# Kernel tuning notes

Hardware: AMD Instinct MI355X
Metric: run time of the kernel (lower is better)

Reference implementation:

```python
import jax, jax.numpy as jnp
import numpy as np

EPS = 1e-07

def setup_inputs() -> dict:
    key = jax.random.key(0)
    kx, kw, kb, ku = jax.random.split(key, 4)
    B, S, D, A = 1024, 512, 200, 100
    x = jax.random.normal(kx, (B, S, D), dtype=jnp.float32)
    W = jax.random.normal(kw, (D, A), dtype=jnp.float32)
    b = jax.random.normal(kb, (A,), dtype=jnp.float32)
    u = jax.random.normal(ku, (A, 1), dtype=jnp.float32)
    return {"x": x, "W": W, "b": b, "u": u}

def reference(x, W, b, u):
    # uit: [B,S,A] = tanh(x @ W + b)
    uit = jnp.tanh(jnp.einsum('bsd,da->bsa', x, W) + b)
    # ait: [B,S] raw scores -> exp -> normalize over seq (faithful: no max-subtract)
    ait = jnp.exp(jnp.einsum('bsa,a->bs', uit, u[:, 0]))
    ait = ait / (jnp.sum(ait, axis=1, keepdims=True) + EPS)
    # weighted sum pool over seq: [B,D]
    return jnp.einsum('bsd,bs->bd', x, ait)
```

## Files before the change

kernel.cpp:

```cpp
#include <hip/hip_runtime.h>
#include <math.h>


typedef _Float16 half8 __attribute__((ext_vector_type(8)));
typedef _Float16 half4_ __attribute__((ext_vector_type(4)));
typedef float float4_ __attribute__((ext_vector_type(4)));

#define B_   1024
#define S_   512
#define D_   200
#define A_   100
#define NPAD 128
#define KPAD 224
#define SC   64
#define NCH  (S_ / SC)
#define PITCH_H 232

#define WT_BYTES (NPAD * KPAD * 2)
#define UB_BYTES (NPAD * 2 * 4)
#define NUM_OFF  (WT_BYTES + UB_BYTES)
#define DEN_OFF  (NUM_OFF + (size_t)B_ * NCH * 4 * D_ * 4)

#define DPP_ADD(v, ctrl)                                                     \
  v += __builtin_bit_cast(float, __builtin_amdgcn_update_dpp(                \
           0, __builtin_bit_cast(int, v), (ctrl), 0xF, 0xF, true))

__global__ void prep_kernel(const float* __restrict__ W,
                            const float* __restrict__ bias,
                            const float* __restrict__ u,
                            void* __restrict__ ws) {
  _Float16* wt = (_Float16*)ws;
  float* upad = (float*)((char*)ws + WT_BYTES);
  float* bpad = upad + NPAD;
  int idx = blockIdx.x * 256 + threadIdx.x;
  if (idx < NPAD * KPAD) {
    int n = idx / KPAD;
    int k = idx % KPAD;
    float v = (n < A_ && k < D_) ? W[k * A_ + n] : 0.f;
    wt[idx] = (_Float16)v;
  }
  if (blockIdx.x == 0 && threadIdx.x < NPAD) {
    int t = threadIdx.x;
    upad[t] = (t < A_) ? u[t] : 0.f;
    bpad[t] = (t < A_) ? bias[t] : 0.f;
  }
}

__global__ __launch_bounds__(256, 4)
void attn_kernel(const float* __restrict__ x,
                 void* __restrict__ ws) {
  __shared__ _Float16 xs[SC * PITCH_H];
  __shared__ float score_part[4][SC];
  __shared__ float e_lds[SC];

  const int blk  = blockIdx.x;
  const int b    = blk >> 3;
  const int chunk= blk & 7;
  const int tid  = threadIdx.x;
  const int lane = tid & 63;
  const int wave = tid >> 6;
  const int lm   = lane & 15;
  const int lq   = lane >> 4;

  const _Float16* wt = (const _Float16*)ws;
  const float* upad = (const float*)((const char*)ws + WT_BYTES);
  const float* bpad = upad + NPAD;
  float* num_out = (float*)((char*)ws + NUM_OFF);
  float* den_out = (float*)((char*)ws + DEN_OFF);

  half8 Bfrag[2][7];
  float ureg[2], breg[2];
#pragma unroll
  for (int nn = 0; nn < 2; ++nn) {
    int a = (2 * wave + nn) * 16 + lm;
#pragma unroll
    for (int k = 0; k < 7; ++k)
      Bfrag[nn][k] = *(const half8*)(wt + (size_t)a * KPAD + k * 32 + lq * 8);
    ureg[nn] = upad[a];
    breg[nn] = bpad[a];
  }

  {
    int c  = tid & 63;
    int r0 = tid >> 6;
    const float* xg = x + ((size_t)b * S_ + (size_t)chunk * SC) * D_;
#pragma unroll
    for (int j = 0; j < 16; ++j) {
      int row = r0 + 4 * j;
      if (c < 50) {
        float4_ v = *(const float4_*)(xg + row * D_ + c * 4);
        half4_ h = {(_Float16)v.x, (_Float16)v.y, (_Float16)v.z, (_Float16)v.w};
        *(half4_*)(&xs[row * PITCH_H + c * 4]) = h;
      } else if (c < 56) {
        half4_ z = {(_Float16)0.f, (_Float16)0.f, (_Float16)0.f, (_Float16)0.f};
        *(half4_*)(&xs[row * PITCH_H + c * 4]) = z;
      }
    }
  }
  __syncthreads();

  float4_ acc[4][2];
#pragma unroll
  for (int m = 0; m < 4; ++m)
#pragma unroll
    for (int nn = 0; nn < 2; ++nn)
      acc[m][nn] = (float4_){0.f, 0.f, 0.f, 0.f};

#pragma unroll
  for (int k = 0; k < 7; ++k) {
#pragma unroll
    for (int m = 0; m < 4; ++m) {
      half8 af = *(const half8*)(&xs[(m * 16 + lm) * PITCH_H + k * 32 + lq * 8]);
#pragma unroll
      for (int nn = 0; nn < 2; ++nn)
        acc[m][nn] = __builtin_amdgcn_mfma_f32_16x16x32_f16(
            af, Bfrag[nn][k], acc[m][nn], 0, 0, 0);
    }
  }

#pragma unroll
  for (int m = 0; m < 4; ++m) {
#pragma unroll
    for (int r = 0; r < 4; ++r) {
      float v = 0.f;
#pragma unroll
      for (int nn = 0; nn < 2; ++nn) {
        float z  = acc[m][nn][r] + breg[nn];
        float az = fabsf(z);
        float ez = __expf(az + az);
        float rc = __builtin_amdgcn_rcpf(ez + 1.f);
        float t  = fmaf(-2.f, rc, 1.f);
        t = copysignf(t, z);
        v = fmaf(t, ureg[nn], v);
      }
      DPP_ADD(v, 0x111);
      DPP_ADD(v, 0x112);
      DPP_ADD(v, 0x114);
      DPP_ADD(v, 0x118);
      if (lm == 15) score_part[wave][m * 16 + lq * 4 + r] = v;
    }
  }
  __syncthreads();

  if (tid < SC) {
    float ssum = score_part[0][tid] + score_part[1][tid] +
                 score_part[2][tid] + score_part[3][tid];
    float e = __expf(ssum);
    e_lds[tid] = e;
    float d = e;
    d += __shfl_xor(d, 1);
    d += __shfl_xor(d, 2);
    d += __shfl_xor(d, 4);
    d += __shfl_xor(d, 8);
    d += __shfl_xor(d, 16);
    d += __shfl_xor(d, 32);
    if (tid == 0) den_out[blk] = d;
  }
  __syncthreads();

  if (lane < 50) {
    float4_ accv = {0.f, 0.f, 0.f, 0.f};
#pragma unroll
    for (int i = 0; i < 16; ++i) {
      int s = wave * 16 + i;
      float e = e_lds[s];
      half4_ h = *(const half4_*)(&xs[s * PITCH_H + lane * 4]);
      accv.x = fmaf(e, (float)h.x, accv.x);
      accv.y = fmaf(e, (float)h.y, accv.y);
      accv.z = fmaf(e, (float)h.z, accv.z);
      accv.w = fmaf(e, (float)h.w, accv.w);
    }
    *(float4_*)(&num_out[((size_t)blk * 4 + wave) * D_ + lane * 4]) = accv;
  }
}

__global__ __launch_bounds__(256)
void reduce_kernel(const void* __restrict__ ws, float* __restrict__ out) {
  const float* num = (const float*)((const char*)ws + NUM_OFF);
  const float* den = (const float*)((const char*)ws + DEN_OFF);
  int b = blockIdx.x;
  int tid = threadIdx.x;
  if (tid < D_) {
    float d = 0.f;
#pragma unroll
    for (int c = 0; c < NCH; ++c) d += den[b * NCH + c];
    float s = 0.f;
#pragma unroll
    for (int j = 0; j < NCH * 4; ++j)
      s += num[((size_t)b * NCH * 4 + j) * D_ + tid];
    out[(size_t)b * D_ + tid] = s / (d + 1e-7f);
  }
}

extern "C" void kernel_launch(void* const* d_in, const int* in_sizes, int n_in,
                              void* d_out, int out_size, void* d_ws, size_t ws_size,
                              hipStream_t stream) {
  const float* x = (const float*)d_in[0];
  const float* W = (const float*)d_in[1];
  const float* b = (const float*)d_in[2];
  const float* u = (const float*)d_in[3];
  float* out = (float*)d_out;

  int prep_elems = NPAD * KPAD;
  int prep_blocks = (prep_elems + 255) / 256;
  prep_kernel<<<prep_blocks, 256, 0, stream>>>(W, b, u, d_ws);
  attn_kernel<<<B_ * NCH, 256, 0, stream>>>(x, d_ws);
  reduce_kernel<<<B_, 256, 0, stream>>>(d_ws, out);
}
```

Before: 587.7 us.

## Drop LDS staging of x and feed MFMA fragments straight from global

The shared-memory fp16 copy of the 64x200 x tile is removed. Each wave now loads its A fragments directly from global fp32 memory and converts them in registers, and the pooling step re-reads x from global in fp32. This cuts the LDS footprint and the staging barrier, which may raise occupancy. In exchange, every wave reads the whole tile, so the block makes four redundant global/L1 reads plus one more read for pooling, using a strided access pattern.

After: 723.7 us. 23.1% more time.

```diff
diff --git a/kernel.cpp b/kernel.cpp
--- a/kernel.cpp
+++ b/kernel.cpp
@@ -3,7 +3,6 @@
 
 
 typedef _Float16 half8 __attribute__((ext_vector_type(8)));
-typedef _Float16 half4_ __attribute__((ext_vector_type(4)));
 typedef float float4_ __attribute__((ext_vector_type(4)));
 
 #define B_   1024
@@ -14,7 +13,6 @@
 #define KPAD 224
 #define SC   64
 #define NCH  (S_ / SC)
-#define PITCH_H 232
 
 #define WT_BYTES (NPAD * KPAD * 2)
 #define UB_BYTES (NPAD * 2 * 4)
@@ -49,7 +47,6 @@
 __global__ __launch_bounds__(256, 4)
 void attn_kernel(const float* __restrict__ x,
                  void* __restrict__ ws) {
-  __shared__ _Float16 xs[SC * PITCH_H];
   __shared__ float score_part[4][SC];
   __shared__ float e_lds[SC];
 
@@ -80,24 +77,7 @@
     breg[nn] = bpad[a];
   }
 
-  {
-    int c  = tid & 63;
-    int r0 = tid >> 6;
-    const float* xg = x + ((size_t)b * S_ + (size_t)chunk * SC) * D_;
-#pragma unroll
-    for (int j = 0; j < 16; ++j) {
-      int row = r0 + 4 * j;
-      if (c < 50) {
-        float4_ v = *(const float4_*)(xg + row * D_ + c * 4);
-        half4_ h = {(_Float16)v.x, (_Float16)v.y, (_Float16)v.z, (_Float16)v.w};
-        *(half4_*)(&xs[row * PITCH_H + c * 4]) = h;
-      } else if (c < 56) {
-        half4_ z = {(_Float16)0.f, (_Float16)0.f, (_Float16)0.f, (_Float16)0.f};
-        *(half4_*)(&xs[row * PITCH_H + c * 4]) = z;
-      }
-    }
-  }
-  __syncthreads();
+  const float* xg = x + ((size_t)b * S_ + (size_t)chunk * SC) * D_;
 
   float4_ acc[4][2];
 #pragma unroll
@@ -110,7 +90,17 @@
   for (int k = 0; k < 7; ++k) {
 #pragma unroll
     for (int m = 0; m < 4; ++m) {
-      half8 af = *(const half8*)(&xs[(m * 16 + lm) * PITCH_H + k * 32 + lq * 8]);
+      half8 af = {(_Float16)0.f, (_Float16)0.f, (_Float16)0.f, (_Float16)0.f,
+                  (_Float16)0.f, (_Float16)0.f, (_Float16)0.f, (_Float16)0.f};
+      if (k < 6 || lq == 0) {
+        const float* p = xg + (m * 16 + lm) * D_ + k * 32 + lq * 8;
+        float4_ lo = *(const float4_*)p;
+        float4_ hi = *(const float4_*)(p + 4);
+        af[0] = (_Float16)lo.x; af[1] = (_Float16)lo.y;
+        af[2] = (_Float16)lo.z; af[3] = (_Float16)lo.w;
+        af[4] = (_Float16)hi.x; af[5] = (_Float16)hi.y;
+        af[6] = (_Float16)hi.z; af[7] = (_Float16)hi.w;
+      }
 #pragma unroll
       for (int nn = 0; nn < 2; ++nn)
         acc[m][nn] = __builtin_amdgcn_mfma_f32_16x16x32_f16(
@@ -164,11 +154,11 @@
     for (int i = 0; i < 16; ++i) {
       int s = wave * 16 + i;
       float e = e_lds[s];
-      half4_ h = *(const half4_*)(&xs[s * PITCH_H + lane * 4]);
-      accv.x = fmaf(e, (float)h.x, accv.x);
-      accv.y = fmaf(e, (float)h.y, accv.y);
-      accv.z = fmaf(e, (float)h.z, accv.z);
-      accv.w = fmaf(e, (float)h.w, accv.w);
+      float4_ v = *(const float4_*)(xg + s * D_ + lane * 4);
+      accv.x = fmaf(e, v.x, accv.x);
+      accv.y = fmaf(e, v.y, accv.y);
+      accv.z = fmaf(e, v.z, accv.z);
+      accv.w = fmaf(e, v.w, accv.w);
     }
     *(float4_*)(&num_out[((size_t)blk * 4 + wave) * D_ + lane * 4]) = accv;
   }
```
